# Performance work log

Measured on AMD Instinct MI355X. Metric: run time of the kernel, lower is better.

The kernel has to match this reference:

```python
import jax, jax.numpy as jnp
import numpy as np

B, N, G = 4096, 20, 4
D_IN, D_OUT, H = 128, 64, 8
LRELU = 0.2  # TF leaky_relu default alpha


def _glorot(key, shape):
    fan_in, fan_out = shape[-2], shape[-1]
    scale = jnp.sqrt(6.0 / (fan_in + fan_out)).astype(jnp.float32)
    return jax.random.uniform(key, shape, jnp.float32, -1.0, 1.0) * scale


def setup_inputs() -> dict:
    key = jax.random.key(0)
    k1, k2, k3, k4, k5, k6 = jax.random.split(key, 6)
    return {
        "self_vecs": jax.random.normal(k1, (B, G, D_IN), jnp.float32),
        "neigh_vecs": jax.random.normal(k2, (B, N, G, D_IN), jnp.float32),
        "W_heads": _glorot(k3, (H, D_IN, D_OUT)),      # per-head before_attend_weights
        "a_self": _glorot(k4, (H, D_OUT, 1))[..., 0],  # per-head attend_weights_self  [H, D_OUT]
        "a_neigh": _glorot(k5, (H, D_OUT, 1))[..., 0], # per-head attend_weights_neigh [H, D_OUT]
        "W_out": _glorot(k6, (H * D_OUT, D_OUT)),      # final FC weights
    }


def reference(self_vecs, neigh_vecs, W_heads, a_self, a_neigh, W_out):
    # Transform self and neighbor vectors for all heads at once.
    self_t = jnp.einsum("bgd,hde->bghe", self_vecs, W_heads)    # [B,G,H,E]
    neigh_t = jnp.einsum("bngd,hde->bnghe", neigh_vecs, W_heads)  # [B,N,G,H,E]

    f_self = jnp.einsum("bghe,he->bgh", self_t, a_self)          # [B,G,H]
    f_neigh = jnp.einsum("bnghe,he->bngh", neigh_t, a_neigh)     # [B,N,G,H]

    # logits [B,N,G,H]; original applies softmax over the num_graphs axis (tf default last axis of [B,N,G])
    logits = f_self[:, None, :, :] + f_neigh
    attend = jax.nn.softmax(jax.nn.leaky_relu(logits, LRELU), axis=2)  # softmax over G

    # Weighted aggregation over neighbors: [B,G,H,E]
    out_h = jnp.einsum("bngh,bnghe->bghe", attend, neigh_t)
    out_h = jax.nn.leaky_relu(out_h, LRELU)  # per-head activation (act=leaky_relu)

    # Concatenate heads along feature dim -> [B,G,H*E], final FC + relu
    h = out_h.reshape(out_h.shape[0], out_h.shape[1], H * D_OUT)
    return jax.nn.relu(jnp.einsum("bgk,ke->bge", h, W_out))
```

## Files before the change

### kernel.cpp

```cpp
#include <hip/hip_runtime.h>
#include <hip/hip_bf16.h>

#define BB 4096
#define NNB 20
#define GG 4
#define DIN 128
#define EE 64
#define HH 8

typedef short bf16x8 __attribute__((ext_vector_type(8)));
typedef float f32x4 __attribute__((ext_vector_type(4)));

__device__ __forceinline__ float lrelu_f(float x) { return x > 0.f ? x : 0.2f * x; }
__device__ __forceinline__ unsigned short f2bf(float f) {
  unsigned u = __float_as_uint(f);
  return (unsigned short)((u + 0x7fffu + ((u >> 16) & 1u)) >> 16);
}
__device__ __forceinline__ float bf2f(unsigned short s) {
  return __uint_as_float(((unsigned)s) << 16);
}

__global__ __launch_bounds__(256) void prep_kernel(
    const float* __restrict__ W_heads, const float* __restrict__ a_self,
    const float* __restrict__ a_neigh, const float* __restrict__ W_out,
    unsigned short* __restrict__ P1Whi, unsigned short* __restrict__ P1Wlo,
    unsigned short* __restrict__ WBhi, unsigned short* __restrict__ WBlo,
    unsigned short* __restrict__ WOhi, unsigned short* __restrict__ WOlo) {
  int id = blockIdx.x * 256 + threadIdx.x;
  if (id < 2048) {
    int j = id & 7, lane = (id >> 3) & 63, kb = id >> 9;
    int col = lane & 15, k = kb * 32 + (lane >> 4) * 8 + j;
    int h = col & 7;
    const float* a = (col < 8) ? a_neigh : a_self;
    const float* Wrow = W_heads + (h * DIN + k) * EE;
    float acc = 0.f;
    for (int e = 0; e < EE; ++e) acc = fmaf(Wrow[e], a[h * EE + e], acc);
    unsigned short hi = f2bf(acc);
    P1Whi[id] = hi;
    P1Wlo[id] = f2bf(acc - bf2f(hi));
  } else if (id < 2048 + 65536) {
    int rel = id - 2048;
    int j = rel & 7, l = (rel >> 3) & 63, kb = (rel >> 9) & 3, nt = (rel >> 11) & 3, h = rel >> 13;
    int d = kb * 32 + (l >> 4) * 8 + j;
    int e = nt * 16 + (l & 15);
    float w = W_heads[(h * DIN + d) * EE + e];
    unsigned short hi = f2bf(w);
    WBhi[rel] = hi;
    WBlo[rel] = f2bf(w - bf2f(hi));
  } else if (id < 2048 + 65536 + 32768) {
    int rel = id - 2048 - 65536;
    int j = rel & 7, l = (rel >> 3) & 63, kb = (rel >> 9) & 15, nt = rel >> 13;
    int k = kb * 32 + (l >> 4) * 8 + j;
    int n = nt * 16 + (l & 15);
    float w = W_out[k * EE + n];
    unsigned short hi = f2bf(w);
    WOhi[rel] = hi;
    WOlo[rel] = f2bf(w - bf2f(hi));
  }
}

__global__ __launch_bounds__(512, 6) void fused_kernel(
    const float* __restrict__ self_vecs, const float* __restrict__ neigh_vecs,
    const unsigned short* __restrict__ P1Whi, const unsigned short* __restrict__ P1Wlo,
    const unsigned short* __restrict__ WBhi, const unsigned short* __restrict__ WBlo,
    const unsigned short* __restrict__ WOhi, const unsigned short* __restrict__ WOlo,
    float* __restrict__ out) {
  __shared__ char smem[53760];
  char* aggb = smem;
  float* fw   = (float*)(smem + 32768);
  float* attw = (float*)(smem + 43520);
  char* hb = smem + 32768;

  const int t = threadIdx.x;
  const int w = t >> 6, lane = t & 63;
  const int m = lane & 15, kg = lane >> 4;
  const int bid = blockIdx.x;

  bf16x8 wfh[4], wfl[4];
#pragma unroll
  for (int kb = 0; kb < 4; ++kb) {
    wfh[kb] = *(const bf16x8*)(P1Whi + (kb * 64 + lane) * 8);
    wfl[kb] = *(const bf16x8*)(P1Wlo + (kb * 64 + lane) * 8);
  }

  const int bl_m = m >> 2, g_m = m & 3;
  for (int tile = w; tile < 21; tile += 8) {
    const float* rowp;
    if (tile < 20)
      rowp = neigh_vecs + (((size_t)(bid * 4 + bl_m) * NNB + tile) * GG + g_m) * DIN;
    else
      rowp = self_vecs + ((size_t)bid * 16 + m) * DIN;
    f32x4 c = {0.f, 0.f, 0.f, 0.f};
#pragma unroll
    for (int kb = 0; kb < 4; ++kb) {
      float4 xa = *(const float4*)(rowp + kb * 32 + kg * 8);
      float4 xb = *(const float4*)(rowp + kb * 32 + kg * 8 + 4);
      float xv[8] = {xa.x, xa.y, xa.z, xa.w, xb.x, xb.y, xb.z, xb.w};
      bf16x8 xh, xl;
#pragma unroll
      for (int j = 0; j < 8; ++j) {
        unsigned short hi = f2bf(xv[j]);
        xh[j] = (short)hi;
        xl[j] = (short)f2bf(xv[j] - bf2f(hi));
      }
      c = __builtin_amdgcn_mfma_f32_16x16x32_bf16(xh, wfh[kb], c, 0, 0, 0);
      c = __builtin_amdgcn_mfma_f32_16x16x32_bf16(xh, wfl[kb], c, 0, 0, 0);
      c = __builtin_amdgcn_mfma_f32_16x16x32_bf16(xl, wfh[kb], c, 0, 0, 0);
    }
    if (tile < 20) {
      if (m < 8) {
#pragma unroll
        for (int reg = 0; reg < 4; ++reg) {
          int row = kg * 4 + reg;
          fw[tile * 128 + ((row * 8 + m) ^ (kg << 3))] = c[reg];
        }
      }
    } else {
      if (m >= 8) {
#pragma unroll
        for (int reg = 0; reg < 4; ++reg) {
          int row = kg * 4 + reg;
          fw[20 * 128 + ((row * 8 + (m - 8)) ^ (kg << 3))] = c[reg];
        }
      }
    }
  }
  __syncthreads();

#pragma unroll
  for (int it = 0; it < 2; ++it) {
    int task = t + it * 512;
    if (task < 640) {
      int bl = task & 3, h = (task >> 2) & 7, n = task >> 5;
      float l[4], mx = -1e30f;
#pragma unroll
      for (int gg = 0; gg < 4; ++gg) {
        int bg = bl * 4 + gg;
        float fn = fw[n * 128 + ((bg * 8 + h) ^ (bl << 3))];
        float fs = fw[20 * 128 + ((bg * 8 + h) ^ (bl << 3))];
        float v = lrelu_f(fs + fn);
        l[gg] = v;
        mx = fmaxf(mx, v);
      }
      float s = 0.f;
#pragma unroll
      for (int gg = 0; gg < 4; ++gg) { l[gg] = __expf(l[gg] - mx); s += l[gg]; }
      float inv = 1.f / s;
#pragma unroll
      for (int gg = 0; gg < 4; ++gg)
        attw[n * 128 + (((bl * 4 + gg) * 8 + h) ^ (bl << 3))] = l[gg] * inv;
    }
  }
  __syncthreads();

#pragma unroll
  for (int i = 0; i < 2; ++i) {
    const int bg = 2 * w + i;
    const int bl = bg >> 2, g = bg & 3;
    const float* nbw = neigh_vecs + ((size_t)(bid * 4 + bl) * NNB * GG + g) * DIN;
    float acc[8][2];
#pragma unroll
    for (int h = 0; h < 8; ++h) { acc[h][0] = 0.f; acc[h][1] = 0.f; }
    for (int n = 0; n < NNB; ++n) {
      float2 x2 = *(const float2*)&nbw[(size_t)n * GG * DIN + 2 * lane];
      const int abase = n * 128 + ((bg * 8) ^ (bl << 3));
      f32x4 a0 = *(const f32x4*)&attw[abase];
      f32x4 a1 = *(const f32x4*)&attw[abase + 4];
#pragma unroll
      for (int h = 0; h < 4; ++h) {
        acc[h][0] = fmaf(a0[h], x2.x, acc[h][0]);
        acc[h][1] = fmaf(a0[h], x2.y, acc[h][1]);
        acc[h + 4][0] = fmaf(a1[h], x2.x, acc[h + 4][0]);
        acc[h + 4][1] = fmaf(a1[h], x2.y, acc[h + 4][1]);
      }
    }
    const int swz = (bg & 7) << 4;
#pragma unroll
    for (int h = 0; h < 8; ++h) {
      unsigned pack = (unsigned)f2bf(acc[h][0]) | ((unsigned)f2bf(acc[h][1]) << 16);
      *(unsigned*)(aggb + ((bg * 2048 + h * 256 + 4 * lane) ^ swz)) = pack;
    }
  }
  __syncthreads();

  {
    const int hh = w;
    const int aswz = (m & 7) << 4;
    bf16x8 a[4];
#pragma unroll
    for (int kb = 0; kb < 4; ++kb)
      a[kb] = *(const bf16x8*)(aggb + ((m * 2048 + hh * 256 + kb * 64 + kg * 16) ^ aswz));
#pragma unroll
    for (int nt = 0; nt < 4; ++nt) {
      f32x4 c = {0.f, 0.f, 0.f, 0.f};
#pragma unroll
      for (int kb = 0; kb < 4; ++kb) {
        const int fi = (((hh * 4 + nt) * 4 + kb) * 64 + lane) * 8;
        bf16x8 bh = *(const bf16x8*)(WBhi + fi);
        bf16x8 bl_ = *(const bf16x8*)(WBlo + fi);
        c = __builtin_amdgcn_mfma_f32_16x16x32_bf16(a[kb], bh, c, 0, 0, 0);
        c = __builtin_amdgcn_mfma_f32_16x16x32_bf16(a[kb], bl_, c, 0, 0, 0);
      }
      const int k = hh * 64 + nt * 16 + m;
#pragma unroll
      for (int reg = 0; reg < 4; ++reg) {
        int row = kg * 4 + reg;
        int byte = (row * 1024 + k * 2) ^ ((row & 7) << 4);
        *(unsigned short*)(hb + byte) = f2bf(lrelu_f(c[reg]));
      }
    }
  }
  __syncthreads();

  if (w < 4) {
    const int nt = w;
    f32x4 acc = {0.f, 0.f, 0.f, 0.f};
    for (int kb = 0; kb < 16; ++kb) {
      int byte = (m * 1024 + (kb * 32 + kg * 8) * 2) ^ ((m & 7) << 4);
      bf16x8 ah = *(const bf16x8*)(hb + byte);
      const int fi = ((nt * 16 + kb) * 64 + lane) * 8;
      bf16x8 bh = *(const bf16x8*)(WOhi + fi);
      bf16x8 bl_ = *(const bf16x8*)(WOlo + fi);
      acc = __builtin_amdgcn_mfma_f32_16x16x32_bf16(ah, bh, acc, 0, 0, 0);
      acc = __builtin_amdgcn_mfma_f32_16x16x32_bf16(ah, bl_, acc, 0, 0, 0);
    }
    const int rbase = bid * 16;
#pragma unroll
    for (int reg = 0; reg < 4; ++reg) {
      int row = rbase + kg * 4 + reg;
      out[(size_t)row * EE + nt * 16 + m] = fmaxf(acc[reg], 0.f);
    }
  }
}

extern "C" void kernel_launch(void* const* d_in, const int* in_sizes, int n_in,
                              void* d_out, int out_size, void* d_ws, size_t ws_size,
                              hipStream_t stream) {
  (void)in_sizes; (void)n_in; (void)out_size; (void)ws_size;
  const float* self_vecs  = (const float*)d_in[0];
  const float* neigh_vecs = (const float*)d_in[1];
  const float* W_heads    = (const float*)d_in[2];
  const float* a_self     = (const float*)d_in[3];
  const float* a_neigh    = (const float*)d_in[4];
  const float* W_out      = (const float*)d_in[5];
  float* out              = (float*)d_out;

  char* ws = (char*)d_ws;
  unsigned short* P1Whi = (unsigned short*)ws;
  unsigned short* P1Wlo = (unsigned short*)(ws + 4096);
  unsigned short* WBhi  = (unsigned short*)(ws + 8192);
  unsigned short* WBlo  = (unsigned short*)(ws + 8192 + 131072);
  unsigned short* WOhi  = (unsigned short*)(ws + 8192 + 262144);
  unsigned short* WOlo  = (unsigned short*)(ws + 8192 + 262144 + 65536);

  prep_kernel<<<(2048 + 65536 + 32768) / 256, 256, 0, stream>>>(
      W_heads, a_self, a_neigh, W_out, P1Whi, P1Wlo, WBhi, WBlo, WOhi, WOlo);

  fused_kernel<<<BB / 4, 512, 0, stream>>>(
      self_vecs, neigh_vecs, P1Whi, P1Wlo, WBhi, WBlo, WOhi, WOlo, out);
}
```

Measured before the change: 82.79 us.

## Fuse attention softmax into projection tiles and stage weight fragments in LDS

Every wave now computes the self-vector projection itself and swaps it between lanes with a shuffle. The softmax over graphs is then done directly in registers right after each neighbor tile's MFMA. This removes the intermediate logit buffer in shared memory, one barrier and the separate softmax pass. The projection weight fragments are loaded once into LDS instead of being held in registers, and total LDS shrinks. The cost is that each of the 8 waves recomputes the self tile, and the MFMA loop now has extra LDS reads.

```diff
diff --git a/kernel.cpp b/kernel.cpp
--- a/kernel.cpp
+++ b/kernel.cpp
@@ -65,10 +65,9 @@
     const unsigned short* __restrict__ WBhi, const unsigned short* __restrict__ WBlo,
     const unsigned short* __restrict__ WOhi, const unsigned short* __restrict__ WOlo,
     float* __restrict__ out) {
-  __shared__ char smem[53760];
+  __shared__ char smem[49152];
   char* aggb = smem;
-  float* fw   = (float*)(smem + 32768);
-  float* attw = (float*)(smem + 43520);
+  float* attw = (float*)(smem + 32768);
   char* hb = smem + 32768;
 
   const int t = threadIdx.x;
@@ -76,69 +75,52 @@
   const int m = lane & 15, kg = lane >> 4;
   const int bid = blockIdx.x;
 
-  bf16x8 wfh[4], wfl[4];
-#pragma unroll
-  for (int kb = 0; kb < 4; ++kb) {
-    wfh[kb] = *(const bf16x8*)(P1Whi + (kb * 64 + lane) * 8);
-    wfl[kb] = *(const bf16x8*)(P1Wlo + (kb * 64 + lane) * 8);
+  if (t < 512) {
+    const float4* src = (t < 256) ? (const float4*)P1Whi : (const float4*)P1Wlo;
+    ((float4*)smem)[t] = src[t & 255];
+  }
+  __syncthreads();
+
+#define P1_TILE(rowp, cvec)                                                    \
+  {                                                                            \
+    _Pragma("unroll") for (int kb = 0; kb < 4; ++kb) {                         \
+      float4 xa = *(const float4*)((rowp) + kb * 32 + kg * 8);                 \
+      float4 xb = *(const float4*)((rowp) + kb * 32 + kg * 8 + 4);             \
+      float xv[8] = {xa.x, xa.y, xa.z, xa.w, xb.x, xb.y, xb.z, xb.w};          \
+      bf16x8 xh, xl;                                                           \
+      _Pragma("unroll") for (int j = 0; j < 8; ++j) {                          \
+        unsigned short hi = f2bf(xv[j]);                                       \
+        xh[j] = (short)hi;                                                     \
+        xl[j] = (short)f2bf(xv[j] - bf2f(hi));                                 \
+      }                                                                        \
+      bf16x8 wh = *(const bf16x8*)(smem + kb * 1024 + lane * 16);              \
+      bf16x8 wl = *(const bf16x8*)(smem + 4096 + kb * 1024 + lane * 16);       \
+      cvec = __builtin_amdgcn_mfma_f32_16x16x32_bf16(xh, wh, cvec, 0, 0, 0);   \
+      cvec = __builtin_amdgcn_mfma_f32_16x16x32_bf16(xh, wl, cvec, 0, 0, 0);   \
+      cvec = __builtin_amdgcn_mfma_f32_16x16x32_bf16(xl, wh, cvec, 0, 0, 0);   \
+    }                                                                          \
+  }
+
+  f32x4 fs;
+  {
+    f32x4 c20 = {0.f, 0.f, 0.f, 0.f};
+    const float* srow = self_vecs + ((size_t)bid * 16 + m) * DIN;
+    P1_TILE(srow, c20)
+#pragma unroll
+    for (int reg = 0; reg < 4; ++reg) fs[reg] = __shfl_xor(c20[reg], 8);
   }
 
   const int bl_m = m >> 2, g_m = m & 3;
-  for (int tile = w; tile < 21; tile += 8) {
-    const float* rowp;
-    if (tile < 20)
-      rowp = neigh_vecs + (((size_t)(bid * 4 + bl_m) * NNB + tile) * GG + g_m) * DIN;
-    else
-      rowp = self_vecs + ((size_t)bid * 16 + m) * DIN;
+  for (int tile = w; tile < 20; tile += 8) {
+    const float* rowp =
+        neigh_vecs + (((size_t)(bid * 4 + bl_m) * NNB + tile) * GG + g_m) * DIN;
     f32x4 c = {0.f, 0.f, 0.f, 0.f};
-#pragma unroll
-    for (int kb = 0; kb < 4; ++kb) {
-      float4 xa = *(const float4*)(rowp + kb * 32 + kg * 8);
-      float4 xb = *(const float4*)(rowp + kb * 32 + kg * 8 + 4);
-      float xv[8] = {xa.x, xa.y, xa.z, xa.w, xb.x, xb.y, xb.z, xb.w};
-      bf16x8 xh, xl;
-#pragma unroll
-      for (int j = 0; j < 8; ++j) {
-        unsigned short hi = f2bf(xv[j]);
-        xh[j] = (short)hi;
-        xl[j] = (short)f2bf(xv[j] - bf2f(hi));
-      }
-      c = __builtin_amdgcn_mfma_f32_16x16x32_bf16(xh, wfh[kb], c, 0, 0, 0);
-      c = __builtin_amdgcn_mfma_f32_16x16x32_bf16(xh, wfl[kb], c, 0, 0, 0);
-      c = __builtin_amdgcn_mfma_f32_16x16x32_bf16(xl, wfh[kb], c, 0, 0, 0);
-    }
-    if (tile < 20) {
-      if (m < 8) {
-#pragma unroll
-        for (int reg = 0; reg < 4; ++reg) {
-          int row = kg * 4 + reg;
-          fw[tile * 128 + ((row * 8 + m) ^ (kg << 3))] = c[reg];
-        }
-      }
-    } else {
-      if (m >= 8) {
-#pragma unroll
-        for (int reg = 0; reg < 4; ++reg) {
-          int row = kg * 4 + reg;
-          fw[20 * 128 + ((row * 8 + (m - 8)) ^ (kg << 3))] = c[reg];
-        }
-      }
-    }
-  }
-  __syncthreads();
-
-#pragma unroll
-  for (int it = 0; it < 2; ++it) {
-    int task = t + it * 512;
-    if (task < 640) {
-      int bl = task & 3, h = (task >> 2) & 7, n = task >> 5;
+    P1_TILE(rowp, c)
+    if (m < 8) {
       float l[4], mx = -1e30f;
 #pragma unroll
       for (int gg = 0; gg < 4; ++gg) {
-        int bg = bl * 4 + gg;
-        float fn = fw[n * 128 + ((bg * 8 + h) ^ (bl << 3))];
-        float fs = fw[20 * 128 + ((bg * 8 + h) ^ (bl << 3))];
-        float v = lrelu_f(fs + fn);
+        float v = lrelu_f(fs[gg] + c[gg]);
         l[gg] = v;
         mx = fmaxf(mx, v);
       }
@@ -148,7 +130,7 @@
       float inv = 1.f / s;
 #pragma unroll
       for (int gg = 0; gg < 4; ++gg)
-        attw[n * 128 + (((bl * 4 + gg) * 8 + h) ^ (bl << 3))] = l[gg] * inv;
+        attw[tile * 128 + (kg * 4 + gg) * 8 + m] = l[gg] * inv;
     }
   }
   __syncthreads();
@@ -163,9 +145,8 @@
     for (int h = 0; h < 8; ++h) { acc[h][0] = 0.f; acc[h][1] = 0.f; }
     for (int n = 0; n < NNB; ++n) {
       float2 x2 = *(const float2*)&nbw[(size_t)n * GG * DIN + 2 * lane];
-      const int abase = n * 128 + ((bg * 8) ^ (bl << 3));
-      f32x4 a0 = *(const f32x4*)&attw[abase];
-      f32x4 a1 = *(const f32x4*)&attw[abase + 4];
+      f32x4 a0 = *(const f32x4*)&attw[n * 128 + bg * 8];
+      f32x4 a1 = *(const f32x4*)&attw[n * 128 + bg * 8 + 4];
 #pragma unroll
       for (int h = 0; h < 4; ++h) {
         acc[h][0] = fmaf(a0[h], x2.x, acc[h][0]);
@@ -231,6 +212,7 @@
       out[(size_t)row * EE + nt * 16 + m] = fmaxf(acc[reg], 0.f);
     }
   }
+#undef P1_TILE
 }
 
 extern "C" void kernel_launch(void* const* d_in, const int* in_sizes, int n_in,
```

Result: faster. 76.45 us (-7.7%).
